# Kernel tuning notes

Hardware: AMD Instinct MI355X
Metric: run time of the kernel (lower is better)

## Reference

```python
import jax, jax.numpy as jnp
import numpy as np

B, N, M, D = 64, 512, 1024, 128

def setup_inputs() -> dict:
    key = jax.random.key(0)
    ks = jax.random.split(key, 7)
    s = 1.0 / np.sqrt(D)
    return {
        "h_c": jax.random.normal(ks[0], (B, N, D), dtype=jnp.float32),
        "h_p": jax.random.normal(ks[1], (B, M, D), dtype=jnp.float32),
        "U_w": jax.random.normal(ks[2], (D, D), dtype=jnp.float32) * s,
        "U_b": jax.random.normal(ks[3], (D,), dtype=jnp.float32) * s,
        "V_w": jax.random.normal(ks[4], (D, D), dtype=jnp.float32) * s,
        "V_b": jax.random.normal(ks[5], (D,), dtype=jnp.float32) * s,
        "q": jax.random.normal(ks[6], (D,), dtype=jnp.float32),
    }

def reference(h_c, h_p, U_w, U_b, V_w, V_b, q):
    # ReLU-activated linear projections (torch Linear: x @ W.T + b)
    Uc = jax.nn.relu(jnp.einsum('bnd,ed->bne', h_c, U_w) + U_b)  # (B,N,D)
    Vp = jax.nn.relu(jnp.einsum('bmd,ed->bme', h_p, V_w) + V_b)  # (B,M,D)
    # bilinear attention scores and softmax over protein axis
    attn = jnp.einsum('bnd,bmd->bnm', Uc, Vp)                    # (B,N,M)
    weights = jax.nn.softmax(attn, axis=-1)
    context = jnp.einsum('bnm,bmd->bnd', weights, Vp)            # (B,N,D)
    joint = (Uc + context) * q                                   # (B,N,D)
    return joint.mean(axis=1)                                    # (B,D)
```

## Files before the change

### kernel.cpp

```cpp
#include <hip/hip_runtime.h>
#include <hip/hip_bf16.h>
#include <cstdint>

#define BB 64
#define NN 512
#define MM 1024
#define DD 128

typedef __bf16 bf16x8 __attribute__((ext_vector_type(8)));
typedef float f32x4 __attribute__((ext_vector_type(4)));

static __device__ __forceinline__ unsigned short f2bf(float f) {
    union { float f; unsigned int i; } v; v.f = f;
    unsigned int x = v.i;
    x += 0x7FFFu + ((x >> 16) & 1u);
    return (unsigned short)(x >> 16);
}
static __device__ __forceinline__ unsigned int f2bf2(float a, float b) {
    union { __hip_bfloat162 h; unsigned int u; } c;
    c.h = __float22bfloat162_rn(make_float2(a, b));
    return c.u;
}
static __device__ __forceinline__ void async16(const void* g, void* l) {
    __builtin_amdgcn_global_load_lds(
        (const __attribute__((address_space(1))) void*)g,
        (__attribute__((address_space(3))) void*)l, 16, 0, 0);
}

__global__ __launch_bounds__(256, 4) void proj_v_kernel(
    const float* __restrict__ X,
    const float* __restrict__ Wv,
    const float* __restrict__ bias,
    unsigned short* __restrict__ Y,
    unsigned short* __restrict__ YT)
{
    __shared__ __align__(16) unsigned short Ws[128 * 136];
    unsigned short* Ys = Ws;
    unsigned short* Ts = Ws + 8192;
    const int t = threadIdx.x;
    const int lane = t & 63;
    const int wave = t >> 6;
    const int n16 = lane & 15, q = lane >> 4;
    const long row0 = (long)blockIdx.x * 64;

    float4 xv[8];
    {
        const float* xrow = X + (row0 + wave * 16 + n16) * DD + q * 8;
        #pragma unroll
        for (int kk = 0; kk < 4; ++kk) {
            xv[2 * kk]     = *(const float4*)(xrow + kk * 32);
            xv[2 * kk + 1] = *(const float4*)(xrow + kk * 32 + 4);
        }
    }

    {
        const float4* Wg = (const float4*)Wv;
        #pragma unroll
        for (int i = 0; i < 16; ++i) {
            int idx = i * 256 + t;
            float4 v = Wg[idx];
            int off = idx * 4;
            uint2 u = { f2bf2(v.x, v.y), f2bf2(v.z, v.w) };
            *(uint2*)&Ws[(off >> 7) * 136 + (off & 127)] = u;
        }
    }
    __syncthreads();

    f32x4 acc[8];
    #pragma unroll
    for (int j = 0; j < 8; ++j) acc[j] = {0.f, 0.f, 0.f, 0.f};

    #pragma unroll
    for (int kk = 0; kk < 4; ++kk) {
        float4 x0 = xv[2 * kk], x1 = xv[2 * kk + 1];
        union { bf16x8 v; unsigned int u[4]; } a;
        a.u[0] = f2bf2(x0.x, x0.y); a.u[1] = f2bf2(x0.z, x0.w);
        a.u[2] = f2bf2(x1.x, x1.y); a.u[3] = f2bf2(x1.z, x1.w);
        #pragma unroll
        for (int j = 0; j < 8; ++j) {
            bf16x8 b = *(const bf16x8*)&Ws[(j * 16 + n16) * 136 + q * 8 + kk * 32];
            acc[j] = __builtin_amdgcn_mfma_f32_16x16x32_bf16(a.v, b, acc[j], 0, 0, 0);
        }
    }

    unsigned short yb[8][4];
    #pragma unroll
    for (int j = 0; j < 8; ++j) {
        const float bv = bias[j * 16 + n16];
        float y[4];
        #pragma unroll
        for (int r = 0; r < 4; ++r) {
            float v = acc[j][r] + bv;
            y[r] = v > 0.f ? v : 0.f;
        }
        uint2 u = { f2bf2(y[0], y[1]), f2bf2(y[2], y[3]) };
        *(uint2*)&yb[j][0] = u;
    }
    __syncthreads();

    #pragma unroll
    for (int j = 0; j < 8; ++j) {
        const int e = j * 16 + n16;
        #pragma unroll
        for (int r = 0; r < 4; ++r)
            Ys[(wave * 16 + q * 4 + r) * 128 + e] = yb[j][r];
        *(uint2*)&Ts[e * 72 + wave * 16 + q * 4] = *(uint2*)&yb[j][0];
    }
    __syncthreads();

    {
        uint4* dstY = (uint4*)(Y + row0 * DD);
        const long b = row0 >> 10;
        const long mt = (row0 & 1023) >> 6;
        uint4* dstT = (uint4*)(YT + ((b * 16 + mt) * 128) * 64);
        #pragma unroll
        for (int i = 0; i < 4; ++i) {
            int idx = i * 256 + t;
            dstY[idx] = ((const uint4*)Ys)[idx];
            int e = idx >> 3, m = (idx & 7) * 8;
            dstT[idx] = *(const uint4*)&Ts[e * 72 + m];
        }
    }
}

__global__ __launch_bounds__(256, 2) void attn_kernel(
    const float* __restrict__ hc,
    const float* __restrict__ Wu,
    const float* __restrict__ Ub,
    const unsigned short* __restrict__ Vp,
    const unsigned short* __restrict__ VpT,
    float* __restrict__ part)
{
    __shared__ __align__(16) unsigned short smem[37376];
    unsigned short* Ws  = smem;
    unsigned short* Ucs = smem + 17408;
    unsigned short* Ps  = smem + 32768;

    const int t = threadIdx.x;
    const int lane = t & 63;
    const int wave = t >> 6;
    const int n16 = lane & 15, q = lane >> 4;

    const int id = blockIdx.x;
    const int xcd = id & 7;
    const int slot = id >> 3;
    const int b = xcd * 8 + (slot >> 3);
    const int nt = slot & 7;

    const unsigned short* vpb = Vp + (long)b * MM * DD;
    const unsigned short* vtb = VpT + (long)b * MM * DD;

    const float LOG2E = 1.44269504088896f;

    {
        const float4* Wg = (const float4*)Wu;
        #pragma unroll
        for (int i = 0; i < 16; ++i) {
            int idx = i * 256 + t;
            float4 v = Wg[idx];
            int off = idx * 4;
            uint2 u = { f2bf2(v.x, v.y), f2bf2(v.z, v.w) };
            *(uint2*)&Ws[(off >> 7) * 136 + (off & 127)] = u;
        }
    }
    __syncthreads();

    f32x4 acc[8];
    #pragma unroll
    for (int j = 0; j < 8; ++j) acc[j] = {0.f, 0.f, 0.f, 0.f};
    {
        const float* xrow = hc + ((long)b * NN + nt * 64 + wave * 16 + n16) * DD + q * 8;
        #pragma unroll
        for (int kk = 0; kk < 4; ++kk) {
            float4 x0 = *(const float4*)(xrow + kk * 32);
            float4 x1 = *(const float4*)(xrow + kk * 32 + 4);
            union { bf16x8 v; unsigned int u[4]; } a;
            a.u[0] = f2bf2(x0.x, x0.y); a.u[1] = f2bf2(x0.z, x0.w);
            a.u[2] = f2bf2(x1.x, x1.y); a.u[3] = f2bf2(x1.z, x1.w);
            #pragma unroll
            for (int j = 0; j < 8; ++j) {
                bf16x8 bb = *(const bf16x8*)&Ws[(j * 16 + n16) * 136 + q * 8 + kk * 32];
                acc[j] = __builtin_amdgcn_mfma_f32_16x16x32_bf16(a.v, bb, acc[j], 0, 0, 0);
            }
        }
    }
    float ucred[8];
    #pragma unroll
    for (int j = 0; j < 8; ++j) {
        const float bv = Ub[j * 16 + n16];
        float s = 0.f;
        #pragma unroll
        for (int r = 0; r < 4; ++r) {
            float v = acc[j][r] + bv;
            v = v > 0.f ? v : 0.f;
            s += v;
            Ucs[(wave * 16 + q * 4 + r) * 136 + j * 16 + n16] = f2bf(v * LOG2E);
        }
        ucred[j] = s;
    }
    __syncthreads();

    bf16x8 Bg[4][4];
    #pragma unroll
    for (int j = 0; j < 4; ++j)
        #pragma unroll
        for (int kk = 0; kk < 4; ++kk)
            Bg[j][kk] = *(const bf16x8*)&Ucs[(j * 16 + n16) * 136 + q * 8 + kk * 32];

    {
        #pragma unroll
        for (int i = 0; i < 4; ++i) {
            int L = wave * 256 + i * 64 + lane;
            int r = L >> 4, sc = L & 15, c = sc ^ (r & 7);
            async16(vpb + r * 128 + c * 8, smem + wave * 2048 + i * 512);
        }
        #pragma unroll
        for (int i = 0; i < 4; ++i) {
            int L = wave * 256 + i * 64 + lane;
            int r = L >> 3, sc = L & 7, c = sc ^ (r & 7);
            async16(vtb + r * 64 + c * 8, smem + 8192 + wave * 2048 + i * 512);
        }
    }
    __syncthreads();

    f32x4 O[8];
    #pragma unroll
    for (int j = 0; j < 8; ++j) O[j] = {0.f, 0.f, 0.f, 0.f};
    float lpart[4] = {0.f, 0.f, 0.f, 0.f};

    for (int mt = 0; mt < 16; ++mt) {
        const unsigned short* Vs  = smem + ((mt & 1) ? 16384 : 0);
        const unsigned short* VTs = Vs + 8192;
        unsigned short* nVs = smem + ((mt & 1) ? 0 : 16384);

        f32x4 S[4];
        #pragma unroll
        for (int j = 0; j < 4; ++j) S[j] = {0.f, 0.f, 0.f, 0.f};
        #pragma unroll
        for (int kk = 0; kk < 4; ++kk) {
            int row = wave * 16 + n16;
            int col = ((kk * 4 + q) ^ (n16 & 7)) * 8;
            bf16x8 a = *(const bf16x8*)&Vs[row * 128 + col];
            #pragma unroll
            for (int j = 0; j < 4; ++j)
                S[j] = __builtin_amdgcn_mfma_f32_16x16x32_bf16(a, Bg[j][kk], S[j], 0, 0, 0);
        }

        #pragma unroll
        for (int j = 0; j < 4; ++j) {
            float p0 = __builtin_exp2f(S[j][0]);
            float p1 = __builtin_exp2f(S[j][1]);
            float p2 = __builtin_exp2f(S[j][2]);
            float p3 = __builtin_exp2f(S[j][3]);
            lpart[j] += (p0 + p1) + (p2 + p3);
            uint2 u = { f2bf2(p0, p1), f2bf2(p2, p3) };
            *(uint2*)&Ps[(j * 16 + n16) * 72 + wave * 16 + q * 4] = u;
        }
        __syncthreads();

        if (mt < 15) {
            const unsigned short* sv = vpb + (mt + 1) * 8192;
            const unsigned short* st = vtb + (mt + 1) * 8192;
            #pragma unroll
            for (int i = 0; i < 4; ++i) {
                int L = wave * 256 + i * 64 + lane;
                int r = L >> 4, sc = L & 15, c = sc ^ (r & 7);
                async16(sv + r * 128 + c * 8, nVs + wave * 2048 + i * 512);
            }
            #pragma unroll
            for (int i = 0; i < 4; ++i) {
                int L = wave * 256 + i * 64 + lane;
                int r = L >> 3, sc = L & 7, c = sc ^ (r & 7);
                async16(st + r * 64 + c * 8, nVs + 8192 + wave * 2048 + i * 512);
            }
        }

        #pragma unroll
        for (int kk = 0; kk < 2; ++kk) {
            bf16x8 a = *(const bf16x8*)&Ps[(wave * 16 + n16) * 72 + kk * 32 + q * 8];
            #pragma unroll
            for (int j = 0; j < 8; ++j) {
                int row = j * 16 + n16;
                int col = ((kk * 4 + q) ^ (n16 & 7)) * 8;
                bf16x8 bb = *(const bf16x8*)&VTs[row * 64 + col];
                O[j] = __builtin_amdgcn_mfma_f32_16x16x32_bf16(a, bb, O[j], 0, 0, 0);
            }
        }
        __syncthreads();
    }

    #pragma unroll
    for (int j = 0; j < 4; ++j) {
        lpart[j] += __shfl_xor(lpart[j], 16);
        lpart[j] += __shfl_xor(lpart[j], 32);
    }
    float* lred = (float*)Ps;
    float* red  = (float*)Ps + 256;
    if (q == 0) {
        #pragma unroll
        for (int j = 0; j < 4; ++j)
            lred[wave * 64 + j * 16 + n16] = lpart[j];
    }
    __syncthreads();

    float inv[4];
    #pragma unroll
    for (int r = 0; r < 4; ++r) {
        int n = wave * 16 + q * 4 + r;
        inv[r] = 1.0f / (lred[n] + lred[64 + n] + lred[128 + n] + lred[192 + n]);
    }

    #pragma unroll
    for (int j = 0; j < 8; ++j) {
        float s = ucred[j]
                + O[j][0] * inv[0] + O[j][1] * inv[1]
                + O[j][2] * inv[2] + O[j][3] * inv[3];
        s += __shfl_xor(s, 16);
        s += __shfl_xor(s, 32);
        if (q == 0)
            red[wave * 128 + j * 16 + n16] = s;
    }
    __syncthreads();
    if (t < 128) {
        float tot = red[t] + red[128 + t] + red[256 + t] + red[384 + t];
        part[(long)(b * 8 + nt) * DD + t] = tot;
    }
}

__global__ __launch_bounds__(256) void finalize_kernel(
    const float* __restrict__ part, const float* __restrict__ qv,
    float* __restrict__ out)
{
    int i = blockIdx.x * 256 + threadIdx.x;
    int b = i >> 7, d = i & 127;
    const float* p = part + (long)b * 8 * DD + d;
    float s = 0.f;
    #pragma unroll
    for (int nt = 0; nt < 8; ++nt) s += p[nt * DD];
    out[i] = s * qv[d] * (1.0f / (float)NN);
}

extern "C" void kernel_launch(void* const* d_in, const int* in_sizes, int n_in,
                              void* d_out, int out_size, void* d_ws, size_t ws_size,
                              hipStream_t stream) {
    const float* h_c = (const float*)d_in[0];
    const float* h_p = (const float*)d_in[1];
    const float* U_w = (const float*)d_in[2];
    const float* U_b = (const float*)d_in[3];
    const float* V_w = (const float*)d_in[4];
    const float* V_b = (const float*)d_in[5];
    const float* qv  = (const float*)d_in[6];
    float* out = (float*)d_out;

    unsigned short* Vp  = (unsigned short*)d_ws;
    unsigned short* VpT = Vp + (size_t)BB * MM * DD;
    float* part = (float*)(VpT + (size_t)BB * MM * DD);

    proj_v_kernel<<<BB * MM / 64, 256, 0, stream>>>(h_p, V_w, V_b, Vp, VpT);
    attn_kernel<<<512, 256, 0, stream>>>(h_c, U_w, U_b, Vp, VpT, part);
    finalize_kernel<<<32, 256, 0, stream>>>(part, qv, out);
}
```

Measured before the change: 130.5 us.

## Keep P in registers and stream V tiles directly from global memory

Restructures the attention loop so each wave reads its V and V^T fragments straight from global memory into registers, prefetching the next tile, instead of double-buffering them through LDS. The softmax probabilities feed the second matmul directly from the first MFMA's output layout through 16x16x16 MFMAs, so the Ps LDS round-trip and the per-tile barriers go away. Each wave now keeps a 4x8 output accumulator and splits work over the M axis, with per-wave partial outputs reduced at the end. This costs far more accumulator registers and uncached-by-LDS global loads, which may hurt occupancy or memory latency hiding.

```diff
diff --git a/kernel.cpp b/kernel.cpp
--- a/kernel.cpp
+++ b/kernel.cpp
@@ -9,6 +9,7 @@
 
 typedef __bf16 bf16x8 __attribute__((ext_vector_type(8)));
 typedef float f32x4 __attribute__((ext_vector_type(4)));
+typedef short s16x4 __attribute__((ext_vector_type(4)));
 
 static __device__ __forceinline__ unsigned short f2bf(float f) {
     union { float f; unsigned int i; } v; v.f = f;
@@ -20,11 +21,6 @@
     union { __hip_bfloat162 h; unsigned int u; } c;
     c.h = __float22bfloat162_rn(make_float2(a, b));
     return c.u;
-}
-static __device__ __forceinline__ void async16(const void* g, void* l) {
-    __builtin_amdgcn_global_load_lds(
-        (const __attribute__((address_space(1))) void*)g,
-        (__attribute__((address_space(3))) void*)l, 16, 0, 0);
 }
 
 __global__ __launch_bounds__(256, 4) void proj_v_kernel(
@@ -123,6 +119,64 @@
     }
 }
 
+static __device__ __forceinline__ void attn_step(
+    int mt,
+    const unsigned short* __restrict__ vpb,
+    const unsigned short* __restrict__ vtb,
+    const unsigned short* Ucs,
+    int a_off, int vt_off, int ucs_off,
+    bf16x8 (&aC)[4], bf16x8 (&aN)[4],
+    f32x4 (&O)[4][8], float (&lpart)[4])
+{
+    s16x4 bf[8];
+    {
+        const unsigned short* tb = vtb + mt * 8192 + vt_off;
+        #pragma unroll
+        for (int dj = 0; dj < 8; ++dj)
+            bf[dj] = *(const s16x4*)(tb + dj * 1024);
+    }
+    {
+        int nx = mt + 1; if (nx > 15) nx = 15;
+        const unsigned short* pa = vpb + nx * 8192 + a_off;
+        #pragma unroll
+        for (int kk = 0; kk < 4; ++kk)
+            aN[kk] = *(const bf16x8*)(pa + kk * 32);
+    }
+
+    f32x4 S[4];
+    #pragma unroll
+    for (int j = 0; j < 4; ++j) S[j] = {0.f, 0.f, 0.f, 0.f};
+    #pragma unroll
+    for (int kk = 0; kk < 4; ++kk) {
+        #pragma unroll
+        for (int j = 0; j < 4; ++j) {
+            bf16x8 bg = *(const bf16x8*)&Ucs[j * (16 * 136) + ucs_off + kk * 32];
+            S[j] = __builtin_amdgcn_mfma_f32_16x16x32_bf16(aC[kk], bg, S[j], 0, 0, 0);
+        }
+    }
+
+    s16x4 av[4];
+    #pragma unroll
+    for (int j = 0; j < 4; ++j) {
+        float p0 = __builtin_exp2f(S[j][0]);
+        float p1 = __builtin_exp2f(S[j][1]);
+        float p2 = __builtin_exp2f(S[j][2]);
+        float p3 = __builtin_exp2f(S[j][3]);
+        lpart[j] += (p0 + p1) + (p2 + p3);
+        union { unsigned int u[2]; s16x4 v; } pk;
+        pk.u[0] = f2bf2(p0, p1); pk.u[1] = f2bf2(p2, p3);
+        av[j] = pk.v;
+    }
+
+    #pragma unroll
+    for (int dj = 0; dj < 8; ++dj) {
+        #pragma unroll
+        for (int j = 0; j < 4; ++j)
+            O[j][dj] = __builtin_amdgcn_mfma_f32_16x16x16bf16_1k(
+                av[j], bf[dj], O[j][dj], 0, 0, 0);
+    }
+}
+
 __global__ __launch_bounds__(256, 2) void attn_kernel(
     const float* __restrict__ hc,
     const float* __restrict__ Wu,
@@ -131,10 +185,9 @@
     const unsigned short* __restrict__ VpT,
     float* __restrict__ part)
 {
-    __shared__ __align__(16) unsigned short smem[37376];
+    __shared__ __align__(16) unsigned short smem[26112];
     unsigned short* Ws  = smem;
     unsigned short* Ucs = smem + 17408;
-    unsigned short* Ps  = smem + 32768;
 
     const int t = threadIdx.x;
     const int lane = t & 63;
@@ -200,93 +253,26 @@
     }
     __syncthreads();
 
-    bf16x8 Bg[4][4];
+    f32x4 O[4][8];
     #pragma unroll
     for (int j = 0; j < 4; ++j)
         #pragma unroll
-        for (int kk = 0; kk < 4; ++kk)
-            Bg[j][kk] = *(const bf16x8*)&Ucs[(j * 16 + n16) * 136 + q * 8 + kk * 32];
-
-    {
-        #pragma unroll
-        for (int i = 0; i < 4; ++i) {
-            int L = wave * 256 + i * 64 + lane;
-            int r = L >> 4, sc = L & 15, c = sc ^ (r & 7);
-            async16(vpb + r * 128 + c * 8, smem + wave * 2048 + i * 512);
-        }
-        #pragma unroll
-        for (int i = 0; i < 4; ++i) {
-            int L = wave * 256 + i * 64 + lane;
-            int r = L >> 3, sc = L & 7, c = sc ^ (r & 7);
-            async16(vtb + r * 64 + c * 8, smem + 8192 + wave * 2048 + i * 512);
-        }
-    }
-    __syncthreads();
-
-    f32x4 O[8];
-    #pragma unroll
-    for (int j = 0; j < 8; ++j) O[j] = {0.f, 0.f, 0.f, 0.f};
+        for (int dj = 0; dj < 8; ++dj) O[j][dj] = {0.f, 0.f, 0.f, 0.f};
     float lpart[4] = {0.f, 0.f, 0.f, 0.f};
 
-    for (int mt = 0; mt < 16; ++mt) {
-        const unsigned short* Vs  = smem + ((mt & 1) ? 16384 : 0);
-        const unsigned short* VTs = Vs + 8192;
-        unsigned short* nVs = smem + ((mt & 1) ? 0 : 16384);
-
-        f32x4 S[4];
-        #pragma unroll
-        for (int j = 0; j < 4; ++j) S[j] = {0.f, 0.f, 0.f, 0.f};
-        #pragma unroll
-        for (int kk = 0; kk < 4; ++kk) {
-            int row = wave * 16 + n16;
-            int col = ((kk * 4 + q) ^ (n16 & 7)) * 8;
-            bf16x8 a = *(const bf16x8*)&Vs[row * 128 + col];
-            #pragma unroll
-            for (int j = 0; j < 4; ++j)
-                S[j] = __builtin_amdgcn_mfma_f32_16x16x32_bf16(a, Bg[j][kk], S[j], 0, 0, 0);
-        }
-
-        #pragma unroll
-        for (int j = 0; j < 4; ++j) {
-            float p0 = __builtin_exp2f(S[j][0]);
-            float p1 = __builtin_exp2f(S[j][1]);
-            float p2 = __builtin_exp2f(S[j][2]);
-            float p3 = __builtin_exp2f(S[j][3]);
-            lpart[j] += (p0 + p1) + (p2 + p3);
-            uint2 u = { f2bf2(p0, p1), f2bf2(p2, p3) };
-            *(uint2*)&Ps[(j * 16 + n16) * 72 + wave * 16 + q * 4] = u;
-        }
-        __syncthreads();
-
-        if (mt < 15) {
-            const unsigned short* sv = vpb + (mt + 1) * 8192;
-            const unsigned short* st = vtb + (mt + 1) * 8192;
-            #pragma unroll
-            for (int i = 0; i < 4; ++i) {
-                int L = wave * 256 + i * 64 + lane;
-                int r = L >> 4, sc = L & 15, c = sc ^ (r & 7);
-                async16(sv + r * 128 + c * 8, nVs + wave * 2048 + i * 512);
-            }
-            #pragma unroll
-            for (int i = 0; i < 4; ++i) {
-                int L = wave * 256 + i * 64 + lane;
-                int r = L >> 3, sc = L & 7, c = sc ^ (r & 7);
-                async16(st + r * 64 + c * 8, nVs + 8192 + wave * 2048 + i * 512);
-            }
-        }
-
-        #pragma unroll
-        for (int kk = 0; kk < 2; ++kk) {
-            bf16x8 a = *(const bf16x8*)&Ps[(wave * 16 + n16) * 72 + kk * 32 + q * 8];
-            #pragma unroll
-            for (int j = 0; j < 8; ++j) {
-                int row = j * 16 + n16;
-                int col = ((kk * 4 + q) ^ (n16 & 7)) * 8;
-                bf16x8 bb = *(const bf16x8*)&VTs[row * 64 + col];
-                O[j] = __builtin_amdgcn_mfma_f32_16x16x32_bf16(a, bb, O[j], 0, 0, 0);
-            }
-        }
-        __syncthreads();
+    const int a_off  = (wave * 16 + n16) * 128 + q * 8;
+    const int vt_off = n16 * 64 + wave * 16 + q * 4;
+    const int ucs_off = n16 * 136 + q * 8;
+
+    bf16x8 aA[4], aB[4];
+    #pragma unroll
+    for (int kk = 0; kk < 4; ++kk)
+        aA[kk] = *(const bf16x8*)&vpb[a_off + kk * 32];
+
+    #pragma unroll 1
+    for (int mt = 0; mt < 16; mt += 2) {
+        attn_step(mt,     vpb, vtb, Ucs, a_off, vt_off, ucs_off, aA, aB, O, lpart);
+        attn_step(mt + 1, vpb, vtb, Ucs, a_off, vt_off, ucs_off, aB, aA, O, lpart);
     }
 
     #pragma unroll
@@ -294,31 +280,38 @@
         lpart[j] += __shfl_xor(lpart[j], 16);
         lpart[j] += __shfl_xor(lpart[j], 32);
     }
-    float* lred = (float*)Ps;
-    float* red  = (float*)Ps + 256;
+    float* lred = (float*)Ws;
+    float* invs = lred + 256;
+    float* red  = lred + 320;
     if (q == 0) {
         #pragma unroll
         for (int j = 0; j < 4; ++j)
             lred[wave * 64 + j * 16 + n16] = lpart[j];
     }
     __syncthreads();
-
-    float inv[4];
-    #pragma unroll
-    for (int r = 0; r < 4; ++r) {
-        int n = wave * 16 + q * 4 + r;
-        inv[r] = 1.0f / (lred[n] + lred[64 + n] + lred[128 + n] + lred[192 + n]);
-    }
-
-    #pragma unroll
-    for (int j = 0; j < 8; ++j) {
-        float s = ucred[j]
-                + O[j][0] * inv[0] + O[j][1] * inv[1]
-                + O[j][2] * inv[2] + O[j][3] * inv[3];
+    if (t < 64)
+        invs[t] = 1.0f / (lred[t] + lred[64 + t] + lred[128 + t] + lred[192 + t]);
+    __syncthreads();
+
+    float iv[4][4];
+    #pragma unroll
+    for (int j = 0; j < 4; ++j)
+        #pragma unroll
+        for (int r = 0; r < 4; ++r)
+            iv[j][r] = invs[j * 16 + q * 4 + r];
+
+    #pragma unroll
+    for (int dj = 0; dj < 8; ++dj) {
+        float s = ucred[dj];
+        #pragma unroll
+        for (int j = 0; j < 4; ++j) {
+            s += O[j][dj][0] * iv[j][0] + O[j][dj][1] * iv[j][1]
+               + O[j][dj][2] * iv[j][2] + O[j][dj][3] * iv[j][3];
+        }
         s += __shfl_xor(s, 16);
         s += __shfl_xor(s, 32);
         if (q == 0)
-            red[wave * 128 + j * 16 + n16] = s;
+            red[wave * 128 + dj * 16 + n16] = s;
     }
     __syncthreads();
     if (t < 128) {
```

New measurement: 169.0 us. +29.6%, slower.

## Load Vp tiles straight to registers and triple-buffer VpT with fine-grained waits

Applied to the files above, without the earlier changes.

The attention loop no longer stages Vp tiles through LDS. Each wave loads its A-operand fragments for the next tile directly from global memory into registers, alternating between two register sets. VpT tiles are triple-buffered in LDS with a prefetch distance of two, and the __syncthreads calls are replaced by explicit s_waitcnt vmcnt/lgkmcnt barriers plus s_setprio around the MFMA blocks. This cuts LDS footprint and traffic and overlaps global loads across iterations. The cost is more registers, uncoalesced-style direct global loads, and fragile hand-counted wait counts.

```diff
diff --git a/kernel.cpp b/kernel.cpp
--- a/kernel.cpp
+++ b/kernel.cpp
@@ -123,6 +123,84 @@
     }
 }
 
+static __device__ __forceinline__ void bar_lgkm() {
+    asm volatile("s_waitcnt lgkmcnt(0)" ::: "memory");
+    __builtin_amdgcn_s_barrier();
+    __builtin_amdgcn_sched_barrier(0);
+}
+static __device__ __forceinline__ void bar_vm8() {
+    asm volatile("s_waitcnt vmcnt(8) lgkmcnt(0)" ::: "memory");
+    __builtin_amdgcn_s_barrier();
+    __builtin_amdgcn_sched_barrier(0);
+}
+
+static __device__ __forceinline__ void attn_iter(
+    int mt, unsigned short* smem, unsigned short* Ps,
+    const unsigned short* __restrict__ vpb,
+    const unsigned short* __restrict__ vtb,
+    int wave, int lane, int n16, int q, int a_off,
+    const bf16x8 (&Bg)[4][4],
+    bf16x8 (&aC)[4], bf16x8 (&aN)[4],
+    f32x4 (&O)[8], float (&lpart)[4])
+{
+    {
+        int nx = mt + 2; if (nx > 15) nx = 15;
+        const unsigned short* st = vtb + nx * 8192;
+        unsigned short* dst = smem + ((mt + 2) % 3) * 8192 + wave * 2048;
+        #pragma unroll
+        for (int i = 0; i < 4; ++i) {
+            int L = wave * 256 + i * 64 + lane;
+            int r = L >> 3, sc = L & 7, c = sc ^ (r & 7);
+            async16(st + r * 64 + c * 8, dst + i * 512);
+        }
+    }
+    {
+        int nx = mt + 1; if (nx > 15) nx = 15;
+        const unsigned short* pa = vpb + nx * 8192 + a_off;
+        #pragma unroll
+        for (int kk = 0; kk < 4; ++kk)
+            aN[kk] = *(const bf16x8*)(pa + kk * 32);
+    }
+
+    f32x4 S[4];
+    #pragma unroll
+    for (int j = 0; j < 4; ++j) S[j] = {0.f, 0.f, 0.f, 0.f};
+    __builtin_amdgcn_s_setprio(1);
+    #pragma unroll
+    for (int kk = 0; kk < 4; ++kk) {
+        #pragma unroll
+        for (int j = 0; j < 4; ++j)
+            S[j] = __builtin_amdgcn_mfma_f32_16x16x32_bf16(aC[kk], Bg[j][kk], S[j], 0, 0, 0);
+    }
+    __builtin_amdgcn_s_setprio(0);
+
+    #pragma unroll
+    for (int j = 0; j < 4; ++j) {
+        float p0 = __builtin_exp2f(S[j][0]);
+        float p1 = __builtin_exp2f(S[j][1]);
+        float p2 = __builtin_exp2f(S[j][2]);
+        float p3 = __builtin_exp2f(S[j][3]);
+        lpart[j] += (p0 + p1) + (p2 + p3);
+        uint2 u = { f2bf2(p0, p1), f2bf2(p2, p3) };
+        *(uint2*)&Ps[(j * 16 + n16) * 72 + wave * 16 + q * 4] = u;
+    }
+    bar_lgkm();
+
+    const unsigned short* VTs = smem + (mt % 3) * 8192;
+    __builtin_amdgcn_s_setprio(1);
+    #pragma unroll
+    for (int kk = 0; kk < 2; ++kk) {
+        bf16x8 a = *(const bf16x8*)&Ps[(wave * 16 + n16) * 72 + kk * 32 + q * 8];
+        #pragma unroll
+        for (int j = 0; j < 8; ++j) {
+            bf16x8 bb = *(const bf16x8*)&VTs[(j * 16 + n16) * 64 + ((kk * 4 + q) ^ (n16 & 7)) * 8];
+            O[j] = __builtin_amdgcn_mfma_f32_16x16x32_bf16(a, bb, O[j], 0, 0, 0);
+        }
+    }
+    __builtin_amdgcn_s_setprio(0);
+    bar_vm8();
+}
+
 __global__ __launch_bounds__(256, 2) void attn_kernel(
     const float* __restrict__ hc,
     const float* __restrict__ Wu,
@@ -131,10 +209,10 @@
     const unsigned short* __restrict__ VpT,
     float* __restrict__ part)
 {
-    __shared__ __align__(16) unsigned short smem[37376];
+    __shared__ __align__(16) unsigned short smem[29184];
     unsigned short* Ws  = smem;
     unsigned short* Ucs = smem + 17408;
-    unsigned short* Ps  = smem + 32768;
+    unsigned short* Ps  = smem + 24576;
 
     const int t = threadIdx.x;
     const int lane = t & 63;
@@ -207,86 +285,35 @@
         for (int kk = 0; kk < 4; ++kk)
             Bg[j][kk] = *(const bf16x8*)&Ucs[(j * 16 + n16) * 136 + q * 8 + kk * 32];
 
-    {
-        #pragma unroll
-        for (int i = 0; i < 4; ++i) {
-            int L = wave * 256 + i * 64 + lane;
-            int r = L >> 4, sc = L & 15, c = sc ^ (r & 7);
-            async16(vpb + r * 128 + c * 8, smem + wave * 2048 + i * 512);
-        }
+    const int a_off = (wave * 16 + n16) * 128 + q * 8;
+    bf16x8 aA[4], aB[4];
+    #pragma unroll
+    for (int kk = 0; kk < 4; ++kk)
+        aA[kk] = *(const bf16x8*)&vpb[a_off + kk * 32];
+    #pragma unroll
+    for (int tt = 0; tt < 2; ++tt) {
+        const unsigned short* st = vtb + tt * 8192;
+        unsigned short* dst = smem + tt * 8192 + wave * 2048;
         #pragma unroll
         for (int i = 0; i < 4; ++i) {
             int L = wave * 256 + i * 64 + lane;
             int r = L >> 3, sc = L & 7, c = sc ^ (r & 7);
-            async16(vtb + r * 64 + c * 8, smem + 8192 + wave * 2048 + i * 512);
-        }
-    }
-    __syncthreads();
+            async16(st + r * 64 + c * 8, dst + i * 512);
+        }
+    }
+    asm volatile("s_waitcnt vmcnt(4) lgkmcnt(0)" ::: "memory");
+    __builtin_amdgcn_s_barrier();
+    __builtin_amdgcn_sched_barrier(0);
 
     f32x4 O[8];
     #pragma unroll
     for (int j = 0; j < 8; ++j) O[j] = {0.f, 0.f, 0.f, 0.f};
     float lpart[4] = {0.f, 0.f, 0.f, 0.f};
 
-    for (int mt = 0; mt < 16; ++mt) {
-        const unsigned short* Vs  = smem + ((mt & 1) ? 16384 : 0);
-        const unsigned short* VTs = Vs + 8192;
-        unsigned short* nVs = smem + ((mt & 1) ? 0 : 16384);
-
-        f32x4 S[4];
-        #pragma unroll
-        for (int j = 0; j < 4; ++j) S[j] = {0.f, 0.f, 0.f, 0.f};
-        #pragma unroll
-        for (int kk = 0; kk < 4; ++kk) {
-            int row = wave * 16 + n16;
-            int col = ((kk * 4 + q) ^ (n16 & 7)) * 8;
-            bf16x8 a = *(const bf16x8*)&Vs[row * 128 + col];
-            #pragma unroll
-            for (int j = 0; j < 4; ++j)
-                S[j] = __builtin_amdgcn_mfma_f32_16x16x32_bf16(a, Bg[j][kk], S[j], 0, 0, 0);
-        }
-
-        #pragma unroll
-        for (int j = 0; j < 4; ++j) {
-            float p0 = __builtin_exp2f(S[j][0]);
-            float p1 = __builtin_exp2f(S[j][1]);
-            float p2 = __builtin_exp2f(S[j][2]);
-            float p3 = __builtin_exp2f(S[j][3]);
-            lpart[j] += (p0 + p1) + (p2 + p3);
-            uint2 u = { f2bf2(p0, p1), f2bf2(p2, p3) };
-            *(uint2*)&Ps[(j * 16 + n16) * 72 + wave * 16 + q * 4] = u;
-        }
-        __syncthreads();
-
-        if (mt < 15) {
-            const unsigned short* sv = vpb + (mt + 1) * 8192;
-            const unsigned short* st = vtb + (mt + 1) * 8192;
-            #pragma unroll
-            for (int i = 0; i < 4; ++i) {
-                int L = wave * 256 + i * 64 + lane;
-                int r = L >> 4, sc = L & 15, c = sc ^ (r & 7);
-                async16(sv + r * 128 + c * 8, nVs + wave * 2048 + i * 512);
-            }
-            #pragma unroll
-            for (int i = 0; i < 4; ++i) {
-                int L = wave * 256 + i * 64 + lane;
-                int r = L >> 3, sc = L & 7, c = sc ^ (r & 7);
-                async16(st + r * 64 + c * 8, nVs + 8192 + wave * 2048 + i * 512);
-            }
-        }
-
-        #pragma unroll
-        for (int kk = 0; kk < 2; ++kk) {
-            bf16x8 a = *(const bf16x8*)&Ps[(wave * 16 + n16) * 72 + kk * 32 + q * 8];
-            #pragma unroll
-            for (int j = 0; j < 8; ++j) {
-                int row = j * 16 + n16;
-                int col = ((kk * 4 + q) ^ (n16 & 7)) * 8;
-                bf16x8 bb = *(const bf16x8*)&VTs[row * 64 + col];
-                O[j] = __builtin_amdgcn_mfma_f32_16x16x32_bf16(a, bb, O[j], 0, 0, 0);
-            }
-        }
-        __syncthreads();
+    #pragma unroll 1
+    for (int mt = 0; mt < 16; mt += 2) {
+        attn_iter(mt,     smem, Ps, vpb, vtb, wave, lane, n16, q, a_off, Bg, aA, aB, O, lpart);
+        attn_iter(mt + 1, smem, Ps, vpb, vtb, wave, lane, n16, q, a_off, Bg, aB, aA, O, lpart);
     }
 
     #pragma unroll
```

Result: slower. 133.7 us (+2.5%).
